# Optimization experiments

Measured on AMD Instinct MI355X. Metric: run time of the kernel, lower is better.

## Reference

```python
import jax, jax.numpy as jnp
import numpy as np

B, T, C, H = 2, 2048, 1024, 16
HS = C // H  # 64
EPS = 1e-5


def layernorm(x, g, b):
    mu = jnp.mean(x, axis=-1, keepdims=True)
    var = jnp.var(x, axis=-1, keepdims=True)
    return (x - mu) * jax.lax.rsqrt(var + EPS) * g + b


def setup_inputs() -> dict:
    key = jax.random.key(0)
    ks = jax.random.split(key, 12)
    s = lambda fan_in: 1.0 / np.sqrt(fan_in)
    inp = {
        'x':  jax.random.normal(ks[0], (B, T, C), dtype=jnp.float32),
        'Wq': jax.random.uniform(ks[1], (H, C, HS), jnp.float32, -s(C), s(C)),
        'Wk': jax.random.uniform(ks[2], (H, C, HS), jnp.float32, -s(C), s(C)),
        'Wv': jax.random.uniform(ks[3], (H, C, HS), jnp.float32, -s(C), s(C)),
        'Wp': jax.random.uniform(ks[4], (C, C), jnp.float32, -s(C), s(C)),
        'bp': jax.random.uniform(ks[5], (C,), jnp.float32, -s(C), s(C)),
        'W1': jax.random.uniform(ks[6], (C, 4 * C), jnp.float32, -s(C), s(C)),
        'b1': jax.random.uniform(ks[7], (4 * C,), jnp.float32, -s(C), s(C)),
        'W2': jax.random.uniform(ks[8], (4 * C, C), jnp.float32, -s(4 * C), s(4 * C)),
        'b2': jax.random.uniform(ks[9], (C,), jnp.float32, -s(4 * C), s(4 * C)),
        'g1': jnp.ones((C,), jnp.float32),
        'be1': jnp.zeros((C,), jnp.float32),
        'g2': jnp.ones((C,), jnp.float32),
        'be2': jnp.zeros((C,), jnp.float32),
    }
    return inp


def block(x, Wq, Wk, Wv, Wp, bp, W1, b1, W2, b2, g1, be1, g2, be2):
    # quirky residual structure: residual is taken from the post-LN tensor
    x = layernorm(x, g1, be1)
    # batched multi-head attention (all heads at once): [B,H,T,HS]
    q = jnp.einsum('btc,hcd->bhtd', x, Wq)
    k = jnp.einsum('btc,hcd->bhtd', x, Wk)
    v = jnp.einsum('btc,hcd->bhtd', x, Wv)
    # NOTE: original scales by full embedding dim C ** -0.5, not head_size
    scores = jnp.einsum('bhtd,bhsd->bhts', q, k) * (C ** -0.5)
    causal = jnp.tril(jnp.ones((T, T), dtype=bool))
    scores = jnp.where(causal, scores, -jnp.inf)
    wei = jax.nn.softmax(scores, axis=-1)  # dropout p=0 in eval
    out = jnp.einsum('bhts,bhsd->bhtd', wei, v)
    out = out.transpose(0, 2, 1, 3).reshape(B, T, C)  # concat heads
    out = out @ Wp + bp
    x = x + out
    x = layernorm(x, g2, be2)
    ff = jax.nn.relu(x @ W1 + b1) @ W2 + b2
    return x + ff


def reference(x, Wq, Wk, Wv, Wp, bp, W1, b1, W2, b2, g1, be1, g2, be2):
    return block(x, Wq, Wk, Wv, Wp, bp, W1, b1, W2, b2, g1, be1, g2, be2)
```

## Files before the change

kernel.cpp:

```cpp
#include <hip/hip_runtime.h>
#include <hip/hip_bf16.h>
#include <cstdint>
#include <cstddef>

typedef __attribute__((ext_vector_type(8))) short short8;
typedef __attribute__((ext_vector_type(4))) float f32x4;
typedef __attribute__((ext_vector_type(16))) float f32x16;
typedef unsigned int u32;
typedef unsigned short u16;

__device__ inline u16 f2b(float x) {
    union { float f; u32 u; } v; v.f = x;
    u32 u = v.u;
    u32 r = (u + 0x7fff + ((u >> 16) & 1)) >> 16;
    return (u16)r;
}
__device__ inline float b2f(u16 h) {
    union { u32 u; float f; } v; v.u = ((u32)h) << 16;
    return v.f;
}
__device__ inline u32 cvtpk(float lo, float hi) {
    u32 r; asm("v_cvt_pk_bf16_f32 %0, %1, %2" : "=v"(r) : "v"(lo), "v"(hi)); return r;
}
__device__ inline float ex2(float x) {
    float r; asm("v_exp_f32 %0, %1" : "=v"(r) : "v"(x)); return r;
}
__device__ inline void gll16(const void* g, void* l) {
    __builtin_amdgcn_global_load_lds(
        (const __attribute__((address_space(1))) void*)g,
        (__attribute__((address_space(3))) void*)l, 16, 0, 0);
}

__global__ __launch_bounds__(256) void repack_qkv_tiled(
    const float* __restrict__ Wq, const float* __restrict__ Wk, const float* __restrict__ Wv,
    u16* __restrict__ out)
{
    __shared__ u16 lds[64 * 72];
    const int tid = threadIdx.x;
    const int c0 = blockIdx.x * 64;
    const int sh = blockIdx.y;
    const int sel = sh >> 4, h = sh & 15;
    const float* W = (sel == 0) ? Wq : (sel == 1) ? Wk : Wv;
    #pragma unroll
    for (int it = 0; it < 4; ++it) {
        int idx = tid + it * 256;
        int c = idx >> 4, d4 = idx & 15;
        float4 v = *reinterpret_cast<const float4*>(&W[((size_t)(h * 1024 + c0 + c)) * 64 + d4 * 4]);
        lds[(d4 * 4 + 0) * 72 + c] = f2b(v.x);
        lds[(d4 * 4 + 1) * 72 + c] = f2b(v.y);
        lds[(d4 * 4 + 2) * 72 + c] = f2b(v.z);
        lds[(d4 * 4 + 3) * 72 + c] = f2b(v.w);
    }
    __syncthreads();
    #pragma unroll
    for (int it = 0; it < 2; ++it) {
        int idx = tid + it * 256;
        int d = idx >> 3, c8 = idx & 7;
        short8 s = *reinterpret_cast<const short8*>(&lds[d * 72 + c8 * 8]);
        *reinterpret_cast<short8*>(&out[((size_t)(sel * 1024 + h * 64 + d)) * 1024 + c0 + c8 * 8]) = s;
    }
}

__global__ __launch_bounds__(256) void trans_tiled(
    const float* __restrict__ in, u16* __restrict__ out, int P, int Q)
{
    __shared__ u16 lds[64 * 72];
    const int tid = threadIdx.x;
    const int p0 = blockIdx.x * 64, q0 = blockIdx.y * 64;
    #pragma unroll
    for (int it = 0; it < 4; ++it) {
        int idx = tid + it * 256;
        int p = idx >> 4, q4 = idx & 15;
        float4 v = *reinterpret_cast<const float4*>(&in[(size_t)(p0 + p) * Q + q0 + q4 * 4]);
        lds[(q4 * 4 + 0) * 72 + p] = f2b(v.x);
        lds[(q4 * 4 + 1) * 72 + p] = f2b(v.y);
        lds[(q4 * 4 + 2) * 72 + p] = f2b(v.z);
        lds[(q4 * 4 + 3) * 72 + p] = f2b(v.w);
    }
    __syncthreads();
    #pragma unroll
    for (int it = 0; it < 2; ++it) {
        int idx = tid + it * 256;
        int q = idx >> 3, p8 = idx & 7;
        short8 s = *reinterpret_cast<const short8*>(&lds[q * 72 + p8 * 8]);
        *reinterpret_cast<short8*>(&out[(size_t)(q0 + q) * P + p0 + p8 * 8]) = s;
    }
}

__global__ __launch_bounds__(256) void vt_kernel(
    const u16* __restrict__ qkv, u16* __restrict__ vt)
{
    __shared__ u16 lds[64 * 72];
    const int tid = threadIdx.x;
    const int s0 = blockIdx.x * 64, h = blockIdx.y, b = blockIdx.z;
    #pragma unroll
    for (int it = 0; it < 2; ++it) {
        int idx = tid + it * 256;
        int s = idx >> 3, d8 = idx & 7;
        short8 kv = *reinterpret_cast<const short8*>(
            &qkv[((size_t)(b * 2048 + s0 + s)) * 3072 + 2048 + h * 64 + d8 * 8]);
        #pragma unroll
        for (int j = 0; j < 8; ++j) lds[(d8 * 8 + j) * 72 + s] = (u16)kv[j];
    }
    __syncthreads();
    #pragma unroll
    for (int it = 0; it < 2; ++it) {
        int idx = tid + it * 256;
        int d = idx >> 3, s8 = idx & 7;
        short8 s = *reinterpret_cast<const short8*>(&lds[d * 72 + s8 * 8]);
        *reinterpret_cast<short8*>(&vt[((size_t)(b * 16 + h) * 64 + d) * 2048 + s0 + s8 * 8]) = s;
    }
}

__global__ __launch_bounds__(256) void ln_kernel(
    const float* __restrict__ x, const float* __restrict__ g, const float* __restrict__ be,
    float* __restrict__ yf, u16* __restrict__ yb)
{
    int row = blockIdx.x;
    const float4 v = reinterpret_cast<const float4*>(x + (size_t)row * 1024)[threadIdx.x];
    float s  = v.x + v.y + v.z + v.w;
    float s2 = v.x * v.x + v.y * v.y + v.z * v.z + v.w * v.w;
    #pragma unroll
    for (int o = 32; o >= 1; o >>= 1) { s += __shfl_xor(s, o); s2 += __shfl_xor(s2, o); }
    __shared__ float red[8];
    int w = threadIdx.x >> 6;
    if ((threadIdx.x & 63) == 0) { red[w] = s; red[4 + w] = s2; }
    __syncthreads();
    s  = red[0] + red[1] + red[2] + red[3];
    s2 = red[4] + red[5] + red[6] + red[7];
    float mu = s * (1.0f / 1024.0f);
    float var = s2 * (1.0f / 1024.0f) - mu * mu;
    float rs = rsqrtf(var + 1e-5f);
    const float4 gg = reinterpret_cast<const float4*>(g)[threadIdx.x];
    const float4 bb = reinterpret_cast<const float4*>(be)[threadIdx.x];
    float4 o;
    o.x = (v.x - mu) * rs * gg.x + bb.x;
    o.y = (v.y - mu) * rs * gg.y + bb.y;
    o.z = (v.z - mu) * rs * gg.z + bb.z;
    o.w = (v.w - mu) * rs * gg.w + bb.w;
    reinterpret_cast<float4*>(yf + (size_t)row * 1024)[threadIdx.x] = o;
    uint2 pk;
    pk.x = (u32)f2b(o.x) | ((u32)f2b(o.y) << 16);
    pk.y = (u32)f2b(o.z) | ((u32)f2b(o.w) << 16);
    reinterpret_cast<uint2*>(yb + (size_t)row * 1024)[threadIdx.x] = pk;
}

template<bool BIAS, bool RELU, bool RESID, bool OUTB>
__global__ __launch_bounds__(256) void gemm_bt(
    const u16* __restrict__ A, int lda,
    const u16* __restrict__ BT, int ldb,
    void* __restrict__ out, int ldo,
    const float* __restrict__ bias,
    const float* __restrict__ resid,
    int K)
{
    __shared__ __align__(16) char smem[64 * 1024];
    const int tid = threadIdx.x;
    const int lane = tid & 63, w = tid >> 6;
    const int wr = w >> 1, wc = w & 1;
    const int l15 = lane & 15, lq = lane >> 4;

    const int nx = gridDim.x;
    const int nwg = nx * gridDim.y;
    int orig = blockIdx.y * nx + blockIdx.x;
    int wgid = orig;
    if ((nwg & 7) == 0) wgid = (orig & 7) * (nwg >> 3) + (orig >> 3);
    const int m0 = (wgid / nx) * 128, n0 = (wgid % nx) * 128;

    auto stage = [&](int kt, int buf) {
        char* As = smem + buf * 32768;
        char* Bs = smem + buf * 32768 + 16384;
        #pragma unroll
        for (int it = 0; it < 4; ++it) {
            int slot = it * 256 + tid;
            int row = slot >> 3, c8 = (slot & 7) ^ (row & 7);
            gll16(A + (size_t)(m0 + row) * lda + kt + c8 * 8, As + (it * 256 + w * 64) * 16);
        }
        #pragma unroll
        for (int it = 0; it < 4; ++it) {
            int slot = it * 256 + tid;
            int row = slot >> 3, c8 = (slot & 7) ^ (row & 7);
            gll16(BT + (size_t)(n0 + row) * ldb + kt + c8 * 8, Bs + (it * 256 + w * 64) * 16);
        }
    };

    f32x4 acc[4][4] = {};
    const int nk = K >> 6;

    stage(0, 0);
    __syncthreads();

    for (int t = 0; t < nk; ++t) {
        const char* As = smem + (t & 1) * 32768;
        const char* Bs = smem + (t & 1) * 32768 + 16384;
        if (t + 1 < nk) stage((t + 1) << 6, (t + 1) & 1);
        #pragma unroll
        for (int kk = 0; kk < 2; ++kk) {
            const int sc = kk * 4 + lq;
            short8 a[4], b[4];
            #pragma unroll
            for (int mi = 0; mi < 4; ++mi) {
                int row = wr * 64 + mi * 16 + l15;
                a[mi] = *reinterpret_cast<const short8*>(As + row * 128 + ((sc ^ (row & 7)) << 4));
            }
            #pragma unroll
            for (int ni = 0; ni < 4; ++ni) {
                int row = wc * 64 + ni * 16 + l15;
                b[ni] = *reinterpret_cast<const short8*>(Bs + row * 128 + ((sc ^ (row & 7)) << 4));
            }
            #pragma unroll
            for (int mi = 0; mi < 4; ++mi)
                #pragma unroll
                for (int ni = 0; ni < 4; ++ni)
                    acc[mi][ni] = __builtin_amdgcn_mfma_f32_16x16x32_bf16(a[mi], b[ni], acc[mi][ni], 0, 0, 0);
        }
        __syncthreads();
    }

    #pragma unroll
    for (int mi = 0; mi < 4; ++mi) {
        #pragma unroll
        for (int ni = 0; ni < 4; ++ni) {
            int col = n0 + wc * 64 + ni * 16 + l15;
            float bv = BIAS ? bias[col] : 0.0f;
            #pragma unroll
            for (int r = 0; r < 4; ++r) {
                int row = m0 + wr * 64 + mi * 16 + lq * 4 + r;
                float v = acc[mi][ni][r] + bv;
                if (RELU) v = v > 0.0f ? v : 0.0f;
                if (RESID) v += resid[(size_t)row * ldo + col];
                if (OUTB) ((u16*)out)[(size_t)row * ldo + col] = f2b(v);
                else      ((float*)out)[(size_t)row * ldo + col] = v;
            }
        }
    }
}

__global__ __launch_bounds__(256, 2) void attn_kernel(
    const u16* __restrict__ qkv, const u16* __restrict__ vt, u16* __restrict__ att)
{
    __shared__ __align__(16) char smem[48 * 1024];
    char* Kb0 = smem;
    char* Kb1 = smem + 8192;
    char* Vb0 = smem + 16384;
    char* Vb1 = smem + 24576;
    char* Ost = smem + 32768;

    const int tid = threadIdx.x, lane = tid & 63, w = tid >> 6;
    const int l31 = lane & 31, hi = lane >> 5;
    const int bh = blockIdx.x;
    const int b = bh >> 4, h = bh & 15;
    const size_t base = (size_t)b * 2048;
    const int kcol = 1024 + h * 64;
    const u16* vtp = vt + (size_t)bh * 64 * 2048;
    const float SC = 0.03125f * 1.44269504f;

    auto stage = [&](int st, char* kb, char* vb) {
        #pragma unroll
        for (int i = 0; i < 2; ++i) {
            int seg = w * 2 + i;
            int slot = seg * 64 + lane;
            int s = slot >> 3, d8p = slot & 7;
            gll16(qkv + (base + st * 64 + s) * 3072 + kcol + ((d8p ^ (s & 7)) * 8),
                  kb + seg * 1024);
            int d = s, s8p = d8p;
            gll16(vtp + (size_t)d * 2048 + st * 64 + ((s8p ^ (d & 7)) * 8),
                  vb + seg * 1024);
        }
    };

    for (int pass = 0; pass < 2; ++pass) {
        const int qbi = pass ? (int)blockIdx.y : 15 - (int)blockIdx.y;
        const int q0w = qbi * 128 + w * 32;
        const int nst = 2 * qbi + 2;
        const int qg = q0w + l31;

        short8 qf[4];
        {
            const u16* qp = qkv + (base + q0w + l31) * 3072 + h * 64 + hi * 8;
            #pragma unroll
            for (int dc = 0; dc < 4; ++dc) {
                short8 q = *reinterpret_cast<const short8*>(qp + dc * 16);
                #pragma unroll
                for (int j = 0; j < 8; j += 2) {
                    u32 pk = cvtpk(b2f((u16)q[j]) * SC, b2f((u16)q[j + 1]) * SC);
                    q[j]     = (short)(pk & 0xffff);
                    q[j + 1] = (short)(pk >> 16);
                }
                qf[dc] = q;
            }
        }

        f32x16 oT[2] = {};
        float m = -1e30f, lsum = 0.0f;

        stage(0, Kb0, Vb0);
        __syncthreads();

        for (int st = 0; st < nst; ++st) {
            char* kb = (st & 1) ? Kb1 : Kb0;
            char* vb = (st & 1) ? Vb1 : Vb0;
            if (st + 1 < nst) stage(st + 1, (st & 1) ? Kb0 : Kb1, (st & 1) ? Vb0 : Vb1);

            f32x16 sa[2] = {};
            #pragma unroll
            for (int dc = 0; dc < 4; ++dc) {
                #pragma unroll
                for (int sb = 0; sb < 2; ++sb) {
                    int s = sb * 32 + l31;
                    int slot = (dc * 2 + hi) ^ (s & 7);
                    short8 kf = *reinterpret_cast<const short8*>(kb + s * 128 + slot * 16);
                    sa[sb] = __builtin_amdgcn_mfma_f32_32x32x16_bf16(kf, qf[dc], sa[sb], 0, 0, 0);
                }
            }

            if (st >= nst - 2) {
                #pragma unroll
                for (int sb = 0; sb < 2; ++sb)
                    #pragma unroll
                    for (int r = 0; r < 16; ++r) {
                        int sg = st * 64 + sb * 32 + (r & 3) + 8 * (r >> 2) + 4 * hi;
                        if (sg > qg) sa[sb][r] = -1e30f;
                    }
            }

            float t8[8];
            #pragma unroll
            for (int i = 0; i < 8; ++i)
                t8[i] = fmaxf(fmaxf(sa[0][i], sa[0][i + 8]), fmaxf(sa[1][i], sa[1][i + 8]));
            float t4a = fmaxf(t8[0], t8[4]), t4b = fmaxf(t8[1], t8[5]);
            float t4c = fmaxf(t8[2], t8[6]), t4d = fmaxf(t8[3], t8[7]);
            float mx = fmaxf(fmaxf(t4a, t4b), fmaxf(t4c, t4d));
            mx = fmaxf(mx, __shfl_xor(mx, 32));

            if (!__all(mx <= m + 8.0f)) {
                float nm = fmaxf(m, mx);
                float sf = ex2(m - nm);
                m = nm;
                lsum *= sf;
                #pragma unroll
                for (int dt = 0; dt < 2; ++dt)
                    #pragma unroll
                    for (int r = 0; r < 16; ++r) oT[dt][r] *= sf;
            }

            #pragma unroll
            for (int sb = 0; sb < 2; ++sb)
                #pragma unroll
                for (int r = 0; r < 16; ++r) sa[sb][r] = ex2(sa[sb][r] - m);
            float s8_[8];
            #pragma unroll
            for (int i = 0; i < 8; ++i)
                s8_[i] = (sa[0][i] + sa[0][i + 8]) + (sa[1][i] + sa[1][i + 8]);
            float s4a = s8_[0] + s8_[4], s4b = s8_[1] + s8_[5];
            float s4c = s8_[2] + s8_[6], s4d = s8_[3] + s8_[7];
            float ps = (s4a + s4b) + (s4c + s4d);
            ps += __shfl_xor(ps, 32);
            lsum += ps;

            u32 pkE[4][2], pkO[4][2];
            #pragma unroll
            for (int sc = 0; sc < 4; ++sc) {
                const int sb = sc >> 1, rb = 8 * (sc & 1);
                #pragma unroll
                for (int c = 0; c < 2; ++c) {
                    pkE[sc][c] = cvtpk(sa[sb][rb + 2 * c], sa[sb][rb + 2 * c + 1]);
                    pkO[sc][c] = cvtpk(sa[sb][rb + 4 + 2 * c], sa[sb][rb + 4 + 2 * c + 1]);
                }
            }

            #pragma unroll
            for (int sc = 0; sc < 4; ++sc) {
                u32 wd[4];
                #pragma unroll
                for (int ww = 0; ww < 4; ++ww) {
                    const int c = ww & 1;
                    u32 own  = hi ? pkO[sc][c] : pkE[sc][c];
                    u32 send = hi ? pkE[sc][c] : pkO[sc][c];
                    u32 ex = (u32)__shfl_xor((int)send, 32);
                    wd[ww] = ((ww >> 1) == hi) ? own : ex;
                }
                union { u32 u[4]; short8 s8; } pb_;
                pb_.u[0] = wd[0]; pb_.u[1] = wd[1]; pb_.u[2] = wd[2]; pb_.u[3] = wd[3];
                #pragma unroll
                for (int dt = 0; dt < 2; ++dt) {
                    int d = dt * 32 + l31;
                    int slot = (sc * 2 + hi) ^ (d & 7);
                    short8 vf = *reinterpret_cast<const short8*>(vb + d * 128 + slot * 16);
                    oT[dt] = __builtin_amdgcn_mfma_f32_32x32x16_bf16(vf, pb_.s8, oT[dt], 0, 0, 0);
                }
            }
            __syncthreads();
        }

        {
            float inv = 1.0f / lsum;
            char* ob = Ost + w * 4096;
            #pragma unroll
            for (int dt = 0; dt < 2; ++dt)
                #pragma unroll
                for (int rp = 0; rp < 8; ++rp) {
                    int r = rp * 2;
                    int d = dt * 32 + (r & 3) + 8 * (r >> 2) + 4 * hi;
                    u32 pk2 = cvtpk(oT[dt][r] * inv, oT[dt][r + 1] * inv);
                    int byte = l31 * 128 + ((((d >> 3) ^ (l31 & 7)) << 4)) + (d & 7) * 2;
                    *reinterpret_cast<u32*>(ob + byte) = pk2;
                }
            int q = lane >> 1, half = lane & 1;
            size_t grow = (base + q0w - w * 32 + (w * 32 + q)) * 1024 + h * 64 + half * 32;
            #pragma unroll
            for (int c = 0; c < 4; ++c) {
                int chunk = half * 4 + c;
                int byte = q * 128 + ((chunk ^ (q & 7)) << 4);
                float4 vv = *reinterpret_cast<const float4*>(ob + byte);
                *reinterpret_cast<float4*>(att + grow + c * 8) = vv;
            }
        }
    }
}

extern "C" void kernel_launch(void* const* d_in, const int* in_sizes, int n_in,
                              void* d_out, int out_size, void* d_ws, size_t ws_size,
                              hipStream_t stream)
{
    const float* x   = (const float*)d_in[0];
    const float* Wq  = (const float*)d_in[1];
    const float* Wk  = (const float*)d_in[2];
    const float* Wv  = (const float*)d_in[3];
    const float* Wp  = (const float*)d_in[4];
    const float* bp  = (const float*)d_in[5];
    const float* W1  = (const float*)d_in[6];
    const float* b1  = (const float*)d_in[7];
    const float* W2  = (const float*)d_in[8];
    const float* b2  = (const float*)d_in[9];
    const float* g1  = (const float*)d_in[10];
    const float* be1 = (const float*)d_in[11];
    const float* g2  = (const float*)d_in[12];
    const float* be2 = (const float*)d_in[13];
    float* out = (float*)d_out;

    char* ws = (char*)d_ws;
    u16*   wqkvT = (u16*)(ws + 0);
    u16*   wpT   = (u16*)(ws + 6291456);
    u16*   w1T   = (u16*)(ws + 8388608);
    u16*   w2T   = (u16*)(ws + 16777216);
    float* xlnF  = (float*)(ws + 25165824);
    u16*   xlnB  = (u16*)(ws + 41943040);
    u16*   qkv   = (u16*)(ws + 50331648);
    float* x2    = (float*)(ws + 50331648);
    u16*   hbuf  = (u16*)(ws + 50331648);
    u16*   attb  = (u16*)(ws + 75497472);
    float* yF    = (float*)(ws + 83886080);
    u16*   vtb   = (u16*)(ws + 83886080);
    u16*   yB    = xlnB;

    repack_qkv_tiled<<<dim3(16, 48), 256, 0, stream>>>(Wq, Wk, Wv, wqkvT);
    trans_tiled<<<dim3(16, 16), 256, 0, stream>>>(Wp, wpT, 1024, 1024);
    trans_tiled<<<dim3(16, 64), 256, 0, stream>>>(W1, w1T, 1024, 4096);
    trans_tiled<<<dim3(64, 16), 256, 0, stream>>>(W2, w2T, 4096, 1024);

    ln_kernel<<<4096, 256, 0, stream>>>(x, g1, be1, xlnF, xlnB);

    gemm_bt<false, false, false, true><<<dim3(24, 32), 256, 0, stream>>>(
        xlnB, 1024, wqkvT, 1024, qkv, 3072, nullptr, nullptr, 1024);

    vt_kernel<<<dim3(32, 16, 2), 256, 0, stream>>>(qkv, vtb);
    attn_kernel<<<dim3(32, 8), 256, 0, stream>>>(qkv, vtb, attb);

    gemm_bt<true, false, true, false><<<dim3(8, 32), 256, 0, stream>>>(
        attb, 1024, wpT, 1024, x2, 1024, bp, xlnF, 1024);

    ln_kernel<<<4096, 256, 0, stream>>>(x2, g2, be2, yF, yB);

    gemm_bt<true, true, false, true><<<dim3(32, 32), 256, 0, stream>>>(
        yB, 1024, w1T, 1024, hbuf, 4096, b1, nullptr, 1024);

    gemm_bt<true, false, true, false><<<dim3(8, 32), 256, 0, stream>>>(
        hbuf, 4096, w2T, 4096, out, 1024, b2, yF, 4096);
}
```

Baseline: 235.8 us.

## Add 256x256-tile GEMM kernel for QKV and FFN1 projections

Adds a 512-thread GEMM kernel that computes 256x256 output tiles with double-buffered 128KB LDS, XOR-swizzled layout and grouped workgroup remapping. It replaces the 128x128 GEMM for the QKV projection and the first FFN matmul. Larger tiles raise arithmetic intensity and cut global/L2 traffic. The cost is fewer workgroups (192 and 256 on a 256-CU part), one block per CU, and heavy register use, so occupancy and tail balance may suffer.

```diff
diff --git a/kernel.cpp b/kernel.cpp
--- a/kernel.cpp
+++ b/kernel.cpp
@@ -236,6 +236,105 @@
     }
 }
 
+template<bool BIAS, bool RELU, bool OUTB>
+__global__ __launch_bounds__(512) void gemm_bt256(
+    const u16* __restrict__ A, int lda,
+    const u16* __restrict__ BT, int ldb,
+    void* __restrict__ out, int ldo,
+    const float* __restrict__ bias,
+    int K)
+{
+    __shared__ __align__(16) char smem[128 * 1024];
+    const int tid = threadIdx.x;
+    const int lane = tid & 63, wid = tid >> 6;
+    const int wm = wid >> 2, wn = wid & 3;
+    const int l15 = lane & 15, lq = lane >> 4;
+
+    const int nx = gridDim.x;
+    const int nwg = nx * gridDim.y;
+    int orig = blockIdx.y * nx + blockIdx.x;
+    int wgid = orig;
+    if ((nwg & 7) == 0) wgid = (orig & 7) * (nwg >> 3) + (orig >> 3);
+    const int m0 = (wgid / nx) * 256, n0 = (wgid % nx) * 256;
+
+    auto stage = [&](int kt, int buf) {
+        char* As = smem + buf * 65536;
+        char* Bs = smem + buf * 65536 + 32768;
+        #pragma unroll
+        for (int i = 0; i < 4; ++i) {
+            int slot = i * 512 + tid;
+            int row = slot >> 3, c8 = (slot & 7) ^ (row & 7);
+            gll16(A + (size_t)(m0 + row) * lda + kt + c8 * 8, As + (i * 512 + wid * 64) * 16);
+        }
+        #pragma unroll
+        for (int i = 0; i < 4; ++i) {
+            int slot = i * 512 + tid;
+            int row = slot >> 3, c8 = (slot & 7) ^ (row & 7);
+            gll16(BT + (size_t)(n0 + row) * ldb + kt + c8 * 8, Bs + (i * 512 + wid * 64) * 16);
+        }
+    };
+
+    f32x4 acc[8][4] = {};
+    const int nk = K >> 6;
+
+    stage(0, 0);
+    asm volatile("s_waitcnt vmcnt(0)" ::: "memory");
+    __builtin_amdgcn_s_barrier();
+
+    for (int t = 0; t < nk; ++t) {
+        const char* As = smem + (t & 1) * 65536;
+        const char* Bs = smem + (t & 1) * 65536 + 32768;
+        if (t + 1 < nk) {
+            stage((t + 1) << 6, (t + 1) & 1);
+            asm volatile("s_waitcnt vmcnt(8)" ::: "memory");
+        } else {
+            asm volatile("s_waitcnt vmcnt(0)" ::: "memory");
+        }
+        __builtin_amdgcn_s_barrier();
+
+        #pragma unroll
+        for (int kk = 0; kk < 2; ++kk) {
+            const int sc = kk * 4 + lq;
+            short8 a[8], b[4];
+            #pragma unroll
+            for (int mi = 0; mi < 8; ++mi) {
+                int row = wm * 128 + mi * 16 + l15;
+                a[mi] = *reinterpret_cast<const short8*>(As + row * 128 + ((sc ^ (row & 7)) << 4));
+            }
+            #pragma unroll
+            for (int ni = 0; ni < 4; ++ni) {
+                int row = wn * 64 + ni * 16 + l15;
+                b[ni] = *reinterpret_cast<const short8*>(Bs + row * 128 + ((sc ^ (row & 7)) << 4));
+            }
+            #pragma unroll
+            for (int mi = 0; mi < 8; ++mi)
+                #pragma unroll
+                for (int ni = 0; ni < 4; ++ni)
+                    acc[mi][ni] = __builtin_amdgcn_mfma_f32_16x16x32_bf16(a[mi], b[ni], acc[mi][ni], 0, 0, 0);
+        }
+
+        asm volatile("" ::: "memory");
+        __builtin_amdgcn_s_barrier();
+    }
+
+    #pragma unroll
+    for (int mi = 0; mi < 8; ++mi) {
+        #pragma unroll
+        for (int ni = 0; ni < 4; ++ni) {
+            int col = n0 + wn * 64 + ni * 16 + l15;
+            float bv = BIAS ? bias[col] : 0.0f;
+            #pragma unroll
+            for (int r = 0; r < 4; ++r) {
+                int row = m0 + wm * 128 + mi * 16 + lq * 4 + r;
+                float v = acc[mi][ni][r] + bv;
+                if (RELU) v = v > 0.0f ? v : 0.0f;
+                if (OUTB) ((u16*)out)[(size_t)row * ldo + col] = f2b(v);
+                else      ((float*)out)[(size_t)row * ldo + col] = v;
+            }
+        }
+    }
+}
+
 __global__ __launch_bounds__(256, 2) void attn_kernel(
     const u16* __restrict__ qkv, const u16* __restrict__ vt, u16* __restrict__ att)
 {
@@ -461,8 +560,8 @@
 
     ln_kernel<<<4096, 256, 0, stream>>>(x, g1, be1, xlnF, xlnB);
 
-    gemm_bt<false, false, false, true><<<dim3(24, 32), 256, 0, stream>>>(
-        xlnB, 1024, wqkvT, 1024, qkv, 3072, nullptr, nullptr, 1024);
+    gemm_bt256<false, false, true><<<dim3(12, 16), 512, 0, stream>>>(
+        xlnB, 1024, wqkvT, 1024, qkv, 3072, nullptr, 1024);
 
     vt_kernel<<<dim3(32, 16, 2), 256, 0, stream>>>(qkv, vtb);
     attn_kernel<<<dim3(32, 8), 256, 0, stream>>>(qkv, vtb, attb);
@@ -472,8 +571,8 @@
 
     ln_kernel<<<4096, 256, 0, stream>>>(x2, g2, be2, yF, yB);
 
-    gemm_bt<true, true, false, true><<<dim3(32, 32), 256, 0, stream>>>(
-        yB, 1024, w1T, 1024, hbuf, 4096, b1, nullptr, 1024);
+    gemm_bt256<true, true, true><<<dim3(16, 16), 512, 0, stream>>>(
+        yB, 1024, w1T, 1024, hbuf, 4096, b1, 1024);
 
     gemm_bt<true, false, true, false><<<dim3(8, 32), 256, 0, stream>>>(
         hbuf, 4096, w2T, 4096, out, 1024, b2, yF, 4096);
```

Measured after the change: 225.7 us. -4.3%, faster.
